# Optimization experiments

Measured on AMD Instinct MI355X. Metric: run time of the kernel, lower is better.

Reference implementation:

```python
import jax, jax.numpy as jnp
import numpy as np

V, D, H, T, S = 50000, 256, 512, 16, 8192
H2 = H // 2
START, END = 0, 1
NEG = -10000.0


def setup_inputs() -> dict:
    key = jax.random.key(0)
    ks = jax.random.split(key, 16)

    def rn(k, shape, scale=0.1):
        return jax.random.normal(k, shape, dtype=jnp.float32) * scale

    sentence = jax.random.randint(ks[0], (S,), 0, V)
    emb = rn(ks[1], (V, D), 1.0)
    w_ih_f = rn(ks[2], (4 * H2, D)); w_hh_f = rn(ks[3], (4 * H2, H2))
    b_f = rn(ks[4], (4 * H2,))  # b_ih + b_hh fused
    w_ih_b = rn(ks[5], (4 * H2, D)); w_hh_b = rn(ks[6], (4 * H2, H2))
    b_b = rn(ks[7], (4 * H2,))
    h0_f = rn(ks[8], (H2,), 1.0); c0_f = rn(ks[9], (H2,), 1.0)
    h0_b = rn(ks[10], (H2,), 1.0); c0_b = rn(ks[11], (H2,), 1.0)
    w_out = rn(ks[12], (T, H)); b_out = rn(ks[13], (T,))
    trans = jax.random.normal(ks[14], (T, T), dtype=jnp.float32)
    # transition[START, :] = -10000 ; transition[:, END] = -10000
    trans = trans.at[START, :].set(NEG).at[:, END].set(NEG)
    return {"sentence": sentence, "emb": emb,
            "w_ih_f": w_ih_f, "w_hh_f": w_hh_f, "b_f": b_f,
            "w_ih_b": w_ih_b, "w_hh_b": w_hh_b, "b_b": b_b,
            "h0_f": h0_f, "c0_f": c0_f, "h0_b": h0_b, "c0_b": c0_b,
            "w_out": w_out, "b_out": b_out, "trans": trans}


def _lstm(pre, w_hh, h0, c0):
    # pre: [S, 4*H2] precomputed input projections (x @ W_ih^T + b)
    def step(carry, pre_t):
        h, c = carry
        g = pre_t + w_hh @ h
        i, f, gg, o = jnp.split(g, 4)  # torch gate order: i, f, g, o
        i = jax.nn.sigmoid(i); f = jax.nn.sigmoid(f)
        gg = jnp.tanh(gg); o = jax.nn.sigmoid(o)
        c = f * c + i * gg
        h = o * jnp.tanh(c)
        return (h, c), h
    _, hs = jax.lax.scan(step, (h0, c0), pre)
    return hs  # [S, H2]


def reference(sentence, emb, w_ih_f, w_hh_f, b_f, w_ih_b, w_hh_b, b_b,
              h0_f, c0_f, h0_b, c0_b, w_out, b_out, trans):
    x = emb[sentence]                               # [S, D]
    pre_f = x @ w_ih_f.T + b_f                      # [S, 4*H2]
    pre_b = x[::-1] @ w_ih_b.T + b_b                # reverse direction
    hs_f = _lstm(pre_f, w_hh_f, h0_f, c0_f)         # [S, H2]
    hs_b = _lstm(pre_b, w_hh_b, h0_b, c0_b)[::-1]   # [S, H2]
    feats = jnp.concatenate([hs_f, hs_b], axis=-1) @ w_out.T + b_out  # [S, T]

    # Viterbi (max-plus DP), vectorized over the tag dimension.
    init = jnp.full((T,), NEG, dtype=feats.dtype).at[START].set(0.0)

    def vit_step(score, emit_t):
        cand = score[None, :] + trans               # [T_next, T_prev]
        best = jnp.argmax(cand, axis=1)             # backpointers [T]
        score = jnp.max(cand, axis=1) + emit_t
        return score, best

    last, back = jax.lax.scan(vit_step, init, feats)  # back: [S, T] int
    final = last + trans[END]                       # [T]
    best_last = jnp.argmax(final)
    path_score = final[best_last]

    # Backtrack: path[S-1] = best_last, path[t-1] = back[t][path[t]]
    def back_step(tag, bp_t):
        return bp_t[tag], tag
    _, path = jax.lax.scan(back_step, best_last, back, reverse=True)
    return path_score, path
```

## Files before the change

kernel.cpp:

```cpp
#include <hip/hip_runtime.h>
#include <math.h>

#define SLEN 8192
#define DIM  256
#define H2N  256
#define G4   1024
#define NTAG 16
#define NEGV (-10000.0f)

#define OFF_PRE_F   0
#define OFF_PRE_B   (SLEN*G4)
#define OFF_HS_F    (2*SLEN*G4)
#define OFF_HS_B    (2*SLEN*G4 + SLEN*H2N)
#define OFF_FEATS   (2*SLEN*G4 + 2*SLEN*H2N)
#define WS_NEEDED   ((size_t)(OFF_FEATS + SLEN*NTAG) * 4)

__global__ __launch_bounds__(256) void gemm_pre(
    const int* __restrict__ sent, const float* __restrict__ emb,
    const float* __restrict__ wf, const float* __restrict__ bf,
    const float* __restrict__ wb, const float* __restrict__ bb,
    float* __restrict__ pre_f, float* __restrict__ pre_b)
{
    const int dir = blockIdx.z;
    const float* w    = dir ? wb : wf;
    const float* bias = dir ? bb : bf;
    float* out        = dir ? pre_b : pre_f;
    const int m0 = blockIdx.x * 64, n0 = blockIdx.y * 64;

    __shared__ float As[64][17];
    __shared__ float Bs[64][17];
    __shared__ int   sidx[64];

    const int tid = threadIdx.x;
    const int tx = tid & 15, ty = tid >> 4;

    if (tid < 64) {
        int m = m0 + tid;
        int pos = dir ? (SLEN - 1 - m) : m;
        sidx[tid] = sent[pos];
    }
    __syncthreads();

    float acc[4][4];
#pragma unroll
    for (int i = 0; i < 4; i++)
#pragma unroll
        for (int j = 0; j < 4; j++) acc[i][j] = 0.f;

    const int lr = tid >> 2, lc = (tid & 3) * 4;

    for (int k0 = 0; k0 < DIM; k0 += 16) {
        float4 av = *(const float4*)(emb + (size_t)sidx[lr] * DIM + k0 + lc);
        float4 bv = *(const float4*)(w + (size_t)(n0 + lr) * DIM + k0 + lc);
        As[lr][lc+0] = av.x; As[lr][lc+1] = av.y; As[lr][lc+2] = av.z; As[lr][lc+3] = av.w;
        Bs[lr][lc+0] = bv.x; Bs[lr][lc+1] = bv.y; Bs[lr][lc+2] = bv.z; Bs[lr][lc+3] = bv.w;
        __syncthreads();
#pragma unroll
        for (int k = 0; k < 16; k++) {
            float a[4], b[4];
#pragma unroll
            for (int i = 0; i < 4; i++) a[i] = As[ty*4+i][k];
#pragma unroll
            for (int j = 0; j < 4; j++) b[j] = Bs[tx*4+j][k];
#pragma unroll
            for (int i = 0; i < 4; i++)
#pragma unroll
                for (int j = 0; j < 4; j++) acc[i][j] += a[i] * b[j];
        }
        __syncthreads();
    }

    float4 b4 = *(const float4*)(bias + n0 + tx*4);
#pragma unroll
    for (int i = 0; i < 4; i++) {
        float4 v;
        v.x = acc[i][0] + b4.x; v.y = acc[i][1] + b4.y;
        v.z = acc[i][2] + b4.z; v.w = acc[i][3] + b4.w;
        *(float4*)(out + (size_t)(m0 + ty*4 + i) * G4 + n0 + tx*4) = v;
    }
}

__device__ __forceinline__ float fast_sigmoid(float x) {
    return 1.f / (1.f + __expf(-x));
}
__device__ __forceinline__ float fast_tanh(float x) {
    float xc = fminf(fmaxf(x, -15.f), 15.f);
    float e = __expf(2.f * xc);
    return (e - 1.f) / (e + 1.f);
}

__global__ __launch_bounds__(64)
__attribute__((amdgpu_waves_per_eu(1, 1)))
void lstm_kernel(
    const float* __restrict__ pre_f, const float* __restrict__ pre_b,
    const float* __restrict__ whh_f, const float* __restrict__ whh_b,
    const float* __restrict__ h0_f, const float* __restrict__ c0_f,
    const float* __restrict__ h0_b, const float* __restrict__ c0_b,
    float* __restrict__ hs_f, float* __restrict__ hs_b)
{
    const int blk = blockIdx.x;
    const int d = blk >> 5, cb = blk & 31;
    const int cell0 = cb * 8;
    const float* pre = d ? pre_b : pre_f;
    const float* whh = d ? whh_b : whh_f;
    const float* h0  = d ? h0_b : h0_f;
    const float* c0  = d ? c0_b : c0_f;
    float* hs        = d ? hs_b : hs_f;

    const int l = threadIdx.x;
    const int r = l >> 1;
    const int half = l & 1;
    const int g = r >> 3, cl = r & 7;
    const int grow = g * 256 + cell0 + cl;

    __shared__ __align__(16) float4 w_pack4[32 * 64];
    __shared__ __align__(16) float  h_lds[256];

    {
        const float4* src = (const float4*)(whh + (size_t)grow * H2N + half * 128);
#pragma unroll
        for (int j = 0; j < 32; j++) w_pack4[j * 64 + l] = src[j];
    }
    ((float4*)h_lds)[l] = ((const float4*)h0)[l];
    float c = (l < 8) ? c0[cell0 + l] : 0.f;
    __syncthreads();

    float4 wreg[32];
#pragma unroll
    for (int j = 0; j < 32; j++) wreg[j] = w_pack4[j * 64 + l];
#pragma unroll
    for (int j = 0; j < 32; j++) {
        asm volatile("" : "+v"(wreg[j].x), "+v"(wreg[j].y),
                          "+v"(wreg[j].z), "+v"(wreg[j].w));
    }

    const float* pre_base = pre + grow;
    float pre_cur = (half == 0) ? pre_base[0] : 0.f;
    const int ai = l & 7;

    for (int t = 0; t < SLEN; t++) {
        float pre_next = (half == 0 && t < SLEN - 1) ? pre_base[(size_t)(t + 1) * G4] : 0.f;

        float a0 = pre_cur, a1 = 0.f, a2 = 0.f, a3 = 0.f;
        const float4* hrow4 = (const float4*)(h_lds + half * 128);
#pragma unroll
        for (int j = 0; j < 32; j++) {
            float4 wv = wreg[j];
            float4 hv = hrow4[j];
            a0 += wv.x * hv.x; a1 += wv.y * hv.y;
            a2 += wv.z * hv.z; a3 += wv.w * hv.w;
        }
        float sum = (a0 + a1) + (a2 + a3);
        sum += __shfl_xor(sum, 1, 64);

        float s_i = __shfl(sum, 2 * ai, 64);
        float s_f = __shfl(sum, 16 + 2 * ai, 64);
        float s_g = __shfl(sum, 32 + 2 * ai, 64);
        float s_o = __shfl(sum, 48 + 2 * ai, 64);

        if (l < 8) {
            float i_ = fast_sigmoid(s_i);
            float f_ = fast_sigmoid(s_f);
            float g_ = fast_tanh(s_g);
            float o_ = fast_sigmoid(s_o);
            c = f_ * c + i_ * g_;
            float h = o_ * fast_tanh(c);
            unsigned hm = __float_as_uint(h) | 1u;
            __hip_atomic_store((unsigned*)hs + (size_t)t * H2N + cell0 + l, hm,
                               __ATOMIC_RELAXED, __HIP_MEMORY_SCOPE_AGENT);
        }

        const unsigned* hsrc = (const unsigned*)hs + (size_t)t * H2N + 4 * l;
        unsigned v0, v1, v2, v3;
        int spin = 0;
        do {
            v0 = __hip_atomic_load(hsrc + 0, __ATOMIC_RELAXED, __HIP_MEMORY_SCOPE_AGENT);
            v1 = __hip_atomic_load(hsrc + 1, __ATOMIC_RELAXED, __HIP_MEMORY_SCOPE_AGENT);
            v2 = __hip_atomic_load(hsrc + 2, __ATOMIC_RELAXED, __HIP_MEMORY_SCOPE_AGENT);
            v3 = __hip_atomic_load(hsrc + 3, __ATOMIC_RELAXED, __HIP_MEMORY_SCOPE_AGENT);
        } while (((v0 & v1 & v2 & v3 & 1u) == 0u) && ++spin < 2000000);

        float4 hv4;
        hv4.x = __uint_as_float(v0); hv4.y = __uint_as_float(v1);
        hv4.z = __uint_as_float(v2); hv4.w = __uint_as_float(v3);
        *(float4*)(h_lds + 4 * l) = hv4;
        __syncthreads();
        pre_cur = pre_next;
    }
}

__global__ __launch_bounds__(256) void feats_kernel(
    const float* __restrict__ hs_f, const float* __restrict__ hs_b,
    const float* __restrict__ w_out, const float* __restrict__ b_out,
    float* __restrict__ feats)
{
    const int rs0 = blockIdx.x * 16;
    const int tid = threadIdx.x;
    const int r = tid >> 4, cc = tid & 15;

    __shared__ float Hs[16][513];
    for (int i = tid; i < 16 * 256; i += 256) {
        int rr = i >> 8, k = i & 255;
        Hs[rr][k]       = hs_f[(size_t)(rs0 + rr) * H2N + k];
        Hs[rr][256 + k] = hs_b[(size_t)(SLEN - 1 - (rs0 + rr)) * H2N + k];
    }
    __syncthreads();

    float acc = 0.f;
    const float* wr = w_out + (size_t)cc * 512;
#pragma unroll 8
    for (int k = 0; k < 512; k++) acc += Hs[r][k] * wr[k];
    feats[(size_t)(rs0 + r) * NTAG + cc] = acc + b_out[cc];
}

__global__ __launch_bounds__(64) void viterbi_kernel(
    const float* __restrict__ feats, const float* __restrict__ trans,
    float* __restrict__ out)
{
    __shared__ unsigned char back_s[SLEN * 8];

    const int lane = threadIdx.x;
    const int nx = lane >> 2, pc = lane & 3;

    float tr[4];
#pragma unroll
    for (int j = 0; j < 4; j++) tr[j] = trans[nx * NTAG + pc * 4 + j];

    float sc = (nx == 0) ? 0.f : NEGV;
    float fe = feats[nx];

    for (int t = 0; t < SLEN; t++) {
        float fe_next = (t < SLEN - 1) ? feats[(size_t)(t + 1) * NTAG + nx] : 0.f;

        float bv; int bi;
#pragma unroll
        for (int j = 0; j < 4; j++) {
            float s = __shfl(sc, 4 * (pc * 4 + j), 64);
            float cand = s + tr[j];
            if (j == 0) { bv = cand; bi = pc * 4; }
            else if (cand > bv) { bv = cand; bi = pc * 4 + j; }
        }
#pragma unroll
        for (int off = 1; off < 4; off <<= 1) {
            float ov = __shfl_xor(bv, off, 64);
            int   oi = __shfl_xor(bi, off, 64);
            if (ov > bv || (ov == bv && oi < bi)) { bv = ov; bi = oi; }
        }
        int bi_part = __shfl(bi, (nx | 1) * 4, 64);
        if (pc == 0 && (nx & 1) == 0)
            back_s[t * 8 + (nx >> 1)] = (unsigned char)((bi & 15) | (bi_part << 4));
        sc = bv + fe;
        fe = fe_next;
    }

    float bestv = 0.f; int besti = 0;
#pragma unroll
    for (int j = 0; j < NTAG; j++) {
        float sj = __shfl(sc, 4 * j, 64);
        float fj = sj + trans[1 * NTAG + j];
        if (j == 0) { bestv = fj; besti = 0; }
        else if (fj > bestv) { bestv = fj; besti = j; }
    }
    __syncthreads();

    if (lane == 0) {
        out[0] = bestv;
        int cur = besti;
        for (int t = SLEN - 1; t >= 1; t--) {
            out[1 + t] = (float)cur;
            unsigned char byte = back_s[t * 8 + (cur >> 1)];
            cur = (cur & 1) ? (byte >> 4) : (byte & 15);
        }
        out[1] = (float)cur;
    }
}

extern "C" void kernel_launch(void* const* d_in, const int* in_sizes, int n_in,
                              void* d_out, int out_size, void* d_ws, size_t ws_size,
                              hipStream_t stream) {
    const int*   sent   = (const int*)d_in[0];
    const float* emb    = (const float*)d_in[1];
    const float* w_ih_f = (const float*)d_in[2];
    const float* w_hh_f = (const float*)d_in[3];
    const float* b_f    = (const float*)d_in[4];
    const float* w_ih_b = (const float*)d_in[5];
    const float* w_hh_b = (const float*)d_in[6];
    const float* b_b    = (const float*)d_in[7];
    const float* h0_f   = (const float*)d_in[8];
    const float* c0_f   = (const float*)d_in[9];
    const float* h0_b   = (const float*)d_in[10];
    const float* c0_b   = (const float*)d_in[11];
    const float* w_out  = (const float*)d_in[12];
    const float* b_out  = (const float*)d_in[13];
    const float* trans  = (const float*)d_in[14];
    float* out = (float*)d_out;

    if (ws_size < WS_NEEDED) return;

    float* ws = (float*)d_ws;
    float* pre_f = ws + OFF_PRE_F;
    float* pre_b = ws + OFF_PRE_B;
    float* hs_f  = ws + OFF_HS_F;
    float* hs_b  = ws + OFF_HS_B;
    float* feats = ws + OFF_FEATS;

    gemm_pre<<<dim3(128, 16, 2), 256, 0, stream>>>(sent, emb, w_ih_f, b_f, w_ih_b, b_b, pre_f, pre_b);
    lstm_kernel<<<64, 64, 0, stream>>>(pre_f, pre_b, w_hh_f, w_hh_b,
                                       h0_f, c0_f, h0_b, c0_b, hs_f, hs_b);
    feats_kernel<<<512, 256, 0, stream>>>(hs_f, hs_b, w_out, b_out, feats);
    viterbi_kernel<<<1, 64, 0, stream>>>(feats, trans, out);
}
```

Before: 21.74 ms.

## Use double-buffered epoch-tagged mailbox for LSTM step sync and vectorize LDS reads

```diff
diff --git a/kernel.cpp b/kernel.cpp
--- a/kernel.cpp
+++ b/kernel.cpp
@@ -13,7 +13,8 @@
 #define OFF_HS_F    (2*SLEN*G4)
 #define OFF_HS_B    (2*SLEN*G4 + SLEN*H2N)
 #define OFF_FEATS   (2*SLEN*G4 + 2*SLEN*H2N)
-#define WS_NEEDED   ((size_t)(OFF_FEATS + SLEN*NTAG) * 4)
+#define OFF_MBOX    (OFF_FEATS + SLEN*NTAG)
+#define WS_NEEDED   ((size_t)(OFF_MBOX + 1024) * 4)
 
 __global__ __launch_bounds__(256) void gemm_pre(
     const int* __restrict__ sent, const float* __restrict__ emb,
@@ -27,8 +28,8 @@
     float* out        = dir ? pre_b : pre_f;
     const int m0 = blockIdx.x * 64, n0 = blockIdx.y * 64;
 
-    __shared__ float As[64][17];
-    __shared__ float Bs[64][17];
+    __shared__ float As[16][68];
+    __shared__ float Bs[16][68];
     __shared__ int   sidx[64];
 
     const int tid = threadIdx.x;
@@ -52,16 +53,15 @@
     for (int k0 = 0; k0 < DIM; k0 += 16) {
         float4 av = *(const float4*)(emb + (size_t)sidx[lr] * DIM + k0 + lc);
         float4 bv = *(const float4*)(w + (size_t)(n0 + lr) * DIM + k0 + lc);
-        As[lr][lc+0] = av.x; As[lr][lc+1] = av.y; As[lr][lc+2] = av.z; As[lr][lc+3] = av.w;
-        Bs[lr][lc+0] = bv.x; Bs[lr][lc+1] = bv.y; Bs[lr][lc+2] = bv.z; Bs[lr][lc+3] = bv.w;
+        As[lc+0][lr] = av.x; As[lc+1][lr] = av.y; As[lc+2][lr] = av.z; As[lc+3][lr] = av.w;
+        Bs[lc+0][lr] = bv.x; Bs[lc+1][lr] = bv.y; Bs[lc+2][lr] = bv.z; Bs[lc+3][lr] = bv.w;
         __syncthreads();
 #pragma unroll
         for (int k = 0; k < 16; k++) {
-            float a[4], b[4];
-#pragma unroll
-            for (int i = 0; i < 4; i++) a[i] = As[ty*4+i][k];
-#pragma unroll
-            for (int j = 0; j < 4; j++) b[j] = Bs[tx*4+j][k];
+            float4 a4 = *(const float4*)&As[k][ty * 4];
+            float4 b4 = *(const float4*)&Bs[k][tx * 4];
+            float a[4] = {a4.x, a4.y, a4.z, a4.w};
+            float b[4] = {b4.x, b4.y, b4.z, b4.w};
 #pragma unroll
             for (int i = 0; i < 4; i++)
 #pragma unroll
@@ -89,14 +89,13 @@
     return (e - 1.f) / (e + 1.f);
 }
 
-__global__ __launch_bounds__(64)
-__attribute__((amdgpu_waves_per_eu(1, 1)))
-void lstm_kernel(
+__global__ __launch_bounds__(64) void lstm_kernel(
     const float* __restrict__ pre_f, const float* __restrict__ pre_b,
     const float* __restrict__ whh_f, const float* __restrict__ whh_b,
     const float* __restrict__ h0_f, const float* __restrict__ c0_f,
     const float* __restrict__ h0_b, const float* __restrict__ c0_b,
-    float* __restrict__ hs_f, float* __restrict__ hs_b)
+    float* __restrict__ hs_f, float* __restrict__ hs_b,
+    unsigned* __restrict__ mbox)
 {
     const int blk = blockIdx.x;
     const int d = blk >> 5, cb = blk & 31;
@@ -125,27 +124,21 @@
     float c = (l < 8) ? c0[cell0 + l] : 0.f;
     __syncthreads();
 
-    float4 wreg[32];
-#pragma unroll
-    for (int j = 0; j < 32; j++) wreg[j] = w_pack4[j * 64 + l];
-#pragma unroll
-    for (int j = 0; j < 32; j++) {
-        asm volatile("" : "+v"(wreg[j].x), "+v"(wreg[j].y),
-                          "+v"(wreg[j].z), "+v"(wreg[j].w));
-    }
-
     const float* pre_base = pre + grow;
     float pre_cur = (half == 0) ? pre_base[0] : 0.f;
     const int ai = l & 7;
+    unsigned* mb_dir = mbox + d * 512;
 
     for (int t = 0; t < SLEN; t++) {
         float pre_next = (half == 0 && t < SLEN - 1) ? pre_base[(size_t)(t + 1) * G4] : 0.f;
+        const unsigned etag = (((unsigned)t >> 1) & 1u) ^ 1u;
+        unsigned* mb = mb_dir + (t & 1) * 256;
 
         float a0 = pre_cur, a1 = 0.f, a2 = 0.f, a3 = 0.f;
         const float4* hrow4 = (const float4*)(h_lds + half * 128);
 #pragma unroll
         for (int j = 0; j < 32; j++) {
-            float4 wv = wreg[j];
+            float4 wv = w_pack4[j * 64 + l];
             float4 hv = hrow4[j];
             a0 += wv.x * hv.x; a1 += wv.y * hv.y;
             a2 += wv.z * hv.z; a3 += wv.w * hv.w;
@@ -165,20 +158,22 @@
             float o_ = fast_sigmoid(s_o);
             c = f_ * c + i_ * g_;
             float h = o_ * fast_tanh(c);
-            unsigned hm = __float_as_uint(h) | 1u;
-            __hip_atomic_store((unsigned*)hs + (size_t)t * H2N + cell0 + l, hm,
+            unsigned hm = (__float_as_uint(h) & ~1u) | etag;
+            __hip_atomic_store(mb + cell0 + l, hm,
                                __ATOMIC_RELAXED, __HIP_MEMORY_SCOPE_AGENT);
-        }
-
-        const unsigned* hsrc = (const unsigned*)hs + (size_t)t * H2N + 4 * l;
+            __builtin_nontemporal_store(hm, (unsigned*)hs + (size_t)t * H2N + cell0 + l);
+        }
+
+        const unsigned* msrc = mb + 4 * l;
         unsigned v0, v1, v2, v3;
         int spin = 0;
         do {
-            v0 = __hip_atomic_load(hsrc + 0, __ATOMIC_RELAXED, __HIP_MEMORY_SCOPE_AGENT);
-            v1 = __hip_atomic_load(hsrc + 1, __ATOMIC_RELAXED, __HIP_MEMORY_SCOPE_AGENT);
-            v2 = __hip_atomic_load(hsrc + 2, __ATOMIC_RELAXED, __HIP_MEMORY_SCOPE_AGENT);
-            v3 = __hip_atomic_load(hsrc + 3, __ATOMIC_RELAXED, __HIP_MEMORY_SCOPE_AGENT);
-        } while (((v0 & v1 & v2 & v3 & 1u) == 0u) && ++spin < 2000000);
+            v0 = __hip_atomic_load(msrc + 0, __ATOMIC_RELAXED, __HIP_MEMORY_SCOPE_AGENT);
+            v1 = __hip_atomic_load(msrc + 1, __ATOMIC_RELAXED, __HIP_MEMORY_SCOPE_AGENT);
+            v2 = __hip_atomic_load(msrc + 2, __ATOMIC_RELAXED, __HIP_MEMORY_SCOPE_AGENT);
+            v3 = __hip_atomic_load(msrc + 3, __ATOMIC_RELAXED, __HIP_MEMORY_SCOPE_AGENT);
+        } while ((((v0 ^ etag) | (v1 ^ etag) | (v2 ^ etag) | (v3 ^ etag)) & 1u)
+                 && ++spin < 2000000);
 
         float4 hv4;
         hv4.x = __uint_as_float(v0); hv4.y = __uint_as_float(v1);
@@ -198,7 +193,7 @@
     const int tid = threadIdx.x;
     const int r = tid >> 4, cc = tid & 15;
 
-    __shared__ float Hs[16][513];
+    __shared__ float Hs[16][516];
     for (int i = tid; i < 16 * 256; i += 256) {
         int rr = i >> 8, k = i & 255;
         Hs[rr][k]       = hs_f[(size_t)(rs0 + rr) * H2N + k];
@@ -208,8 +203,14 @@
 
     float acc = 0.f;
     const float* wr = w_out + (size_t)cc * 512;
-#pragma unroll 8
-    for (int k = 0; k < 512; k++) acc += Hs[r][k] * wr[k];
+    const float* hrow = Hs[r];
+#pragma unroll 4
+    for (int kq = 0; kq < 128; kq++) {
+        float4 hv = *(const float4*)(hrow + 4 * kq);
+        float4 wv = *(const float4*)(wr + 4 * kq);
+        acc += hv.x * wv.x; acc += hv.y * wv.y;
+        acc += hv.z * wv.z; acc += hv.w * wv.w;
+    }
     feats[(size_t)(rs0 + r) * NTAG + cc] = acc + b_out[cc];
 }
 
@@ -303,10 +304,11 @@
     float* hs_f  = ws + OFF_HS_F;
     float* hs_b  = ws + OFF_HS_B;
     float* feats = ws + OFF_FEATS;
+    unsigned* mbox = (unsigned*)(ws + OFF_MBOX);
 
     gemm_pre<<<dim3(128, 16, 2), 256, 0, stream>>>(sent, emb, w_ih_f, b_f, w_ih_b, b_b, pre_f, pre_b);
     lstm_kernel<<<64, 64, 0, stream>>>(pre_f, pre_b, w_hh_f, w_hh_b,
-                                       h0_f, c0_f, h0_b, c0_b, hs_f, hs_b);
+                                       h0_f, c0_f, h0_b, c0_b, hs_f, hs_b, mbox);
     feats_kernel<<<512, 256, 0, stream>>>(hs_f, hs_b, w_out, b_out, feats);
     viterbi_kernel<<<1, 64, 0, stream>>>(feats, trans, out);
 }
```

Result: faster. 21.19 ms (-2.5%).
